# Optimization experiments

Hardware: AMD Instinct MI355X
Metric: run time of the kernel (lower is better)

The kernel has to match this reference:

```python
import jax, jax.numpy as jnp
import numpy as np

N_NODES = 50000
N_EDGES = 800000
IN_CH = 128
OUT_CH = 128
TIME_DIM = 64


def setup_inputs() -> dict:
    key = jax.random.key(0)
    ks = jax.random.split(key, 7)
    x = jax.random.normal(ks[0], (N_NODES, IN_CH), dtype=jnp.float32)
    edge_index = jax.random.randint(ks[1], (2, N_EDGES), 0, N_NODES, dtype=jnp.int64)
    edge_t = jax.random.uniform(ks[2], (N_EDGES,), dtype=jnp.float32)
    # parameters
    freqs = jax.random.normal(ks[3], (TIME_DIM // 2,), dtype=jnp.float32)
    fan = IN_CH + TIME_DIM
    lim = float(np.sqrt(1.0 / fan))
    lin_w = jax.random.uniform(ks[4], (OUT_CH, fan), minval=-lim, maxval=lim, dtype=jnp.float32)
    lin_b = jax.random.uniform(ks[5], (OUT_CH,), minval=-lim, maxval=lim, dtype=jnp.float32)
    glim = float(np.sqrt(6.0 / (1 + OUT_CH)))
    attn = jax.random.uniform(ks[6], (1, OUT_CH), minval=-glim, maxval=glim, dtype=jnp.float32)
    return {"x": x, "edge_index": edge_index, "edge_t": edge_t,
            "freqs": freqs, "lin_w": lin_w, "lin_b": lin_b, "attn": attn}


def reference(x, edge_index, edge_t, freqs, lin_w, lin_b, attn):
    src, dst = edge_index[0], edge_index[1]
    n_nodes = x.shape[0]
    # time encoding: [E, time_dim]
    ang = edge_t[:, None] * freqs * (2.0 * jnp.pi)
    edge_attr = jnp.concatenate([jnp.sin(ang), jnp.cos(ang)], axis=-1)
    # gather source features and project: h = tanh(Linear(cat(x_j, te)))
    msg = jnp.concatenate([x[src], edge_attr], axis=-1)        # [E, in+time]
    h = jnp.tanh(msg @ lin_w.T + lin_b)                        # [E, out]
    # segment softmax over destination nodes
    alpha = (h * attn).sum(axis=-1)                            # [E]
    seg_max = jax.ops.segment_max(alpha, dst, num_segments=n_nodes)
    ex = jnp.exp(alpha - seg_max[dst])
    denom = jax.ops.segment_sum(ex, dst, num_segments=n_nodes)
    w = ex / (denom[dst] + 1e-16)
    # scatter-add aggregation
    out = jax.ops.segment_sum(h * w[:, None], dst, num_segments=n_nodes)
    return out
```

## Files before the change

kernel.cpp:

```cpp
#include <hip/hip_runtime.h>
#include <hip/hip_bf16.h>
#include <math.h>

#define IN_CHN 128
#define OUT_CHN 128
#define KD 192
#define TM 64
#define HXP 136

typedef __bf16 bf16x8 __attribute__((ext_vector_type(8)));
typedef float f32x4 __attribute__((ext_vector_type(4)));

static __device__ __forceinline__ unsigned short f2b(float f) {
    return __builtin_bit_cast(unsigned short, (__bf16)f);
}
static __device__ __forceinline__ float b2f(unsigned short b) {
    return __uint_as_float(((unsigned int)b) << 16);
}
static __device__ __forceinline__ float fast_tanh(float x) {
    float e = __expf(2.0f * x);
    return 1.0f - 2.0f * __builtin_amdgcn_rcpf(e + 1.0f);
}

#define GLL16(gsrc, ldst) \
    __builtin_amdgcn_global_load_lds( \
        (const __attribute__((address_space(1))) unsigned int*)(gsrc), \
        (__attribute__((address_space(3))) unsigned int*)(ldst), 16, 0, 0)

#define LDS_BARRIER() do { \
    asm volatile("s_waitcnt lgkmcnt(0)" ::: "memory"); \
    __builtin_amdgcn_s_barrier(); \
    __builtin_amdgcn_sched_barrier(0); \
} while (0)


__global__ __launch_bounds__(256) void cvt_init(const float* __restrict__ x,
    unsigned short* __restrict__ xb, int* __restrict__ deg,
    int* __restrict__ side_node, long long n8, int Nn, int nb)
{
    long long i = (long long)blockIdx.x * 256 + threadIdx.x;
    if (i < n8) {
        const float4* src = (const float4*)(x + i * 8);
        float4 v0 = src[0], v1 = src[1];
        ushort4 p0 = { f2b(v0.x), f2b(v0.y), f2b(v0.z), f2b(v0.w) };
        ushort4 p1 = { f2b(v1.x), f2b(v1.y), f2b(v1.z), f2b(v1.w) };
        *(ushort4*)(xb + i * 8)     = p0;
        *(ushort4*)(xb + i * 8 + 4) = p1;
    }
    int t = (int)i;
    if (t < Nn) deg[t] = 0;
    if (t < nb) side_node[t] = -1;
}


__global__ __launch_bounds__(256) void count_deg(const int* __restrict__ ei,
                                                 int* __restrict__ deg, int E) {
    int e = blockIdx.x * 256 + threadIdx.x;
    if (e < E) atomicAdd(&deg[ei[E + e]], 1);
}

static __device__ __forceinline__ int wave_incl_scan(int v, int lane) {
    #pragma unroll
    for (int off = 1; off < 64; off <<= 1) {
        int t = __shfl_up(v, off);
        if (lane >= off) v += t;
    }
    return v;
}

__global__ __launch_bounds__(256) void scan_local(const int* __restrict__ deg,
    int* __restrict__ offs, int* __restrict__ partial, int Nn)
{
    __shared__ int wsum[4];
    int tid = threadIdx.x, lane = tid & 63, wid = tid >> 6;
    int i = blockIdx.x * 256 + tid;
    int v = (i < Nn) ? deg[i] : 0;
    int incl = wave_incl_scan(v, lane);
    if (lane == 63) wsum[wid] = incl;
    __syncthreads();
    int wpre = 0;
    for (int w = 0; w < wid; ++w) wpre += wsum[w];
    if (i < Nn) offs[i] = wpre + incl - v;
    if (tid == 255) partial[blockIdx.x] = wpre + incl;
}

__global__ __launch_bounds__(256) void finalize2(int* __restrict__ offs,
    const int* __restrict__ partial, int* __restrict__ cursor,
    int Nn, int E, int nblk)
{
    __shared__ int wsum[4];
    int b = blockIdx.x, tid = threadIdx.x, lane = tid & 63, wid = tid >> 6;
    int v = (tid < b && tid < nblk) ? partial[tid] : 0;
    #pragma unroll
    for (int off = 32; off > 0; off >>= 1) v += __shfl_xor(v, off);
    if (lane == 0) wsum[wid] = v;
    __syncthreads();
    int bp = wsum[0] + wsum[1] + wsum[2] + wsum[3];
    int i = b * 256 + tid;
    if (i < Nn) {
        int o = offs[i] + bp;
        offs[i] = o; cursor[i] = o;
        if (i == Nn - 1) offs[Nn] = E;
    }
}

__global__ __launch_bounds__(256) void fill_perm(const int* __restrict__ ei,
    const float* __restrict__ et, int* __restrict__ cursor,
    uint2* __restrict__ mt, int E)
{
    int e = blockIdx.x * 256 + threadIdx.x;
    if (e < E) {
        int d = ei[E + e];
        int pos = atomicAdd(&cursor[d], 1);
        mt[pos] = make_uint2((unsigned)ei[e], __float_as_uint(et[e]));
    }
}


__device__ __forceinline__ void load_meta(const uint2* __restrict__ mt,
    int tile, int E, int rbase, int g, int trow, int sv[2], float& tsv)
{
    int e0 = tile * TM;
    #pragma unroll
    for (int i = 0; i < 2; ++i) {
        int e = e0 + rbase + i * 4 + g;
        sv[i] = (int)mt[e < E ? e : E - 1].x;
    }
    int el = e0 + trow;
    tsv = __uint_as_float(mt[el < E ? el : E - 1].y);
}

__global__ __launch_bounds__(512) void gemm_fused(
    const unsigned short* __restrict__ xb, const uint2* __restrict__ mt,
    const int* __restrict__ offs,
    const float* __restrict__ freqs, const float* __restrict__ lw,
    const float* __restrict__ lb, const float* __restrict__ attn,
    float* __restrict__ out, float* __restrict__ den_g,
    int* __restrict__ side_node, float* __restrict__ side_den,
    float* __restrict__ side_val,
    int E, int Nn, int n_tiles, int kq, int kr)
{
    __shared__ unsigned short xs[2][TM][128];
    __shared__ __align__(16) unsigned short uni[TM * HXP + 128];
    unsigned short* te = uni;
    unsigned short* hx = uni;
    float* exs = (float*)(uni + TM * HXP);

    const int b    = blockIdx.x;
    const int t0   = b * kq + min(b, kr);
    const int cnt  = kq + (b < kr ? 1 : 0);
    if (cnt <= 0 || t0 >= n_tiles) return;
    const int tend = min(t0 + cnt, n_tiles);
    const int be0  = t0 * TM;
    const int bend = min(tend * TM, E);

    const int tid  = threadIdx.x;
    const int lane = tid & 63;
    const int wv   = tid >> 6;
    const int c16  = lane & 15;
    const int g    = lane >> 4;
    const int wbase = wv * 16;
    const int rbase = wv * 8;
    const int trow  = tid >> 3;
    const int tpart = tid & 7;
    const int sub  = lane >> 4;
    const int chl  = lane & 15;

    bf16x8 Wf[6];
    #pragma unroll
    for (int kk = 0; kk < 6; ++kk) {
        const float* wp = lw + (size_t)(wbase + c16) * KD + kk * 32 + g * 8;
        float4 v0 = *(const float4*)wp;
        float4 v1 = *(const float4*)(wp + 4);
        bf16x8 bb;
        bb[0] = (__bf16)v0.x; bb[1] = (__bf16)v0.y; bb[2] = (__bf16)v0.z; bb[3] = (__bf16)v0.w;
        bb[4] = (__bf16)v1.x; bb[5] = (__bf16)v1.y; bb[6] = (__bf16)v1.z; bb[7] = (__bf16)v1.w;
        Wf[kk] = bb;
    }
    const f32x4 bias_v = *(const f32x4*)(lb   + wbase + g * 4);
    const f32x4 attn_v = *(const f32x4*)(attn + wbase + g * 4);

    const float coff = (tpart >= 4) ? 1.5707963267948966f : 0.0f;
    float frv[8];
    #pragma unroll
    for (int j = 0; j < 8; ++j) frv[j] = freqs[(tpart & 3) * 8 + j] * 6.283185307179586f;

    int n0;
    {
        int lo = 0, hi = Nn;
        while (lo + 1 < hi) {
            int mid = (lo + hi) >> 1;
            if (offs[mid] <= be0) lo = mid; else hi = mid;
        }
        n0 = lo;
    }
    int cur_node = n0 + ((wv - (n0 & 7)) & 7);
    float a[8];
    #pragma unroll
    for (int q = 0; q < 8; ++q) a[q] = 0.0f;
    float den = 0.0f;

    float ts_cur, ts_nxt;
    int sv_nxt[2];
    {
        int sv0[2];
        load_meta(mt, t0, E, rbase, g, trow, sv0, ts_cur);
        #pragma unroll
        for (int i = 0; i < 2; ++i) {
            const int rlo = (rbase + i * 4 + g) & 15;
            const unsigned short* gsrc = xb + (size_t)sv0[i] * IN_CHN + ((c16 ^ rlo) * 8);
            GLL16(gsrc, &xs[0][rbase + i * 4][0]);
        }
        int t1 = t0 + 1;
        load_meta(mt, t1 < tend ? t1 : tend - 1, E, rbase, g, trow, sv_nxt, ts_nxt);
    }

    int cur = 0;
    for (int tile = t0; tile < tend; ++tile) {
        const int e0 = tile * TM;
        const int e1 = e0 + TM;

        ushort4 tp[2];
        {
            float v[8];
            #pragma unroll
            for (int j = 0; j < 8; ++j)
                v[j] = __sinf(ts_cur * frv[j] + coff);
            tp[0] = (ushort4){ f2b(v[0]), f2b(v[1]), f2b(v[2]), f2b(v[3]) };
            tp[1] = (ushort4){ f2b(v[4]), f2b(v[5]), f2b(v[6]), f2b(v[7]) };
        }
        int sv2[2]; float ts2;
        {
            int t2 = tile + 2;
            load_meta(mt, t2 < tend ? t2 : tend - 1, E, rbase, g, trow, sv2, ts2);
        }

        __syncthreads();

        if (tile + 1 < tend) {
            #pragma unroll
            for (int i = 0; i < 2; ++i) {
                const int rlo = (rbase + i * 4 + g) & 15;
                const unsigned short* gsrc = xb + (size_t)sv_nxt[i] * IN_CHN + ((c16 ^ rlo) * 8);
                GLL16(gsrc, &xs[cur ^ 1][rbase + i * 4][0]);
            }
        }
        {
            unsigned short* tr = &te[trow * 64];
            int slot = (tpart ^ (trow & 7)) * 8;
            *(ushort4*)(tr + slot)     = tp[0];
            *(ushort4*)(tr + slot + 4) = tp[1];
            if (tid < TM) exs[tid] = 0.0f;
        }

        LDS_BARRIER();

        f32x4 acc[4];
        #pragma unroll
        for (int mi = 0; mi < 4; ++mi) acc[mi] = (f32x4){0.f, 0.f, 0.f, 0.f};

        __builtin_amdgcn_s_setprio(1);
        const unsigned short* xsc = &xs[cur][0][0];
        #pragma unroll
        for (int mi = 0; mi < 4; ++mi) {
            const int r = mi * 16 + c16;
            const unsigned short* xrow = xsc + r * 128;
            #pragma unroll
            for (int kk = 0; kk < 4; ++kk) {
                const int slot = ((kk << 2) + g) ^ c16;
                bf16x8 av = __builtin_bit_cast(bf16x8, *(const uint4*)(xrow + slot * 8));
                acc[mi] = __builtin_amdgcn_mfma_f32_16x16x32_bf16(Wf[kk], av, acc[mi], 0, 0, 0);
            }
            const unsigned short* trw = &te[r * 64];
            bf16x8 s8 = __builtin_bit_cast(bf16x8, *(const uint4*)(trw + ((g ^ (r & 7)) * 8)));
            bf16x8 c8 = __builtin_bit_cast(bf16x8, *(const uint4*)(trw + (((g + 4) ^ (r & 7)) * 8)));
            acc[mi] = __builtin_amdgcn_mfma_f32_16x16x32_bf16(Wf[4], s8, acc[mi], 0, 0, 0);
            acc[mi] = __builtin_amdgcn_mfma_f32_16x16x32_bf16(Wf[5], c8, acc[mi], 0, 0, 0);
        }
        __builtin_amdgcn_s_setprio(0);

        LDS_BARRIER();

        #pragma unroll
        for (int mi = 0; mi < 4; ++mi) {
            const int r = mi * 16 + c16;
            f32x4 z = acc[mi];
            float p = 0.0f;
            #pragma unroll
            for (int q = 0; q < 4; ++q) {
                float h = fast_tanh(z[q] + bias_v[q]);
                z[q] = h;
                p = fmaf(h, attn_v[q], p);
            }
            ushort4 pv = (ushort4){ f2b(z[0]), f2b(z[1]), f2b(z[2]), f2b(z[3]) };
            *(ushort4*)&hx[r * HXP + wbase + g * 4] = pv;
            p += __shfl_xor(p, 16);
            p += __shfl_xor(p, 32);
            if (g == 0) atomicAdd(&exs[r], p);
        }

        LDS_BARRIER();

        while (cur_node < Nn) {
            int s  = offs[cur_node];
            if (s >= e1) break;
            int en = offs[cur_node + 1];
            int lo = s > e0 ? s : e0;
            int hi = en < e1 ? en : e1;
            for (int i = lo + sub; i < hi; i += 4) {
                int li = i - e0;
                float ex = __expf(exs[li]);
                uint4 hv = *(const uint4*)&hx[li * HXP + chl * 8];
                den += ex;
                unsigned int hw[4] = { hv.x, hv.y, hv.z, hv.w };
                #pragma unroll
                for (int q = 0; q < 4; ++q) {
                    a[2*q]   = fmaf(ex, b2f((unsigned short)(hw[q] & 0xFFFFu)), a[2*q]);
                    a[2*q+1] = fmaf(ex, b2f((unsigned short)(hw[q] >> 16)),     a[2*q+1]);
                }
            }
            if (en <= e1) {
                #pragma unroll
                for (int q = 0; q < 8; ++q) {
                    a[q] += __shfl_xor(a[q], 16);
                    a[q] += __shfl_xor(a[q], 32);
                }
                float ds = den + __shfl_xor(den, 16);
                ds += __shfl_xor(ds, 32);
                if (sub == 0) {
                    float* op = out + (size_t)cur_node * OUT_CHN + chl * 8;
                    *(float4*)op       = (float4){a[0], a[1], a[2], a[3]};
                    *(float4*)(op + 4) = (float4){a[4], a[5], a[6], a[7]};
                    if (chl == 0) den_g[cur_node] = ds;
                }
                #pragma unroll
                for (int q = 0; q < 8; ++q) a[q] = 0.0f;
                den = 0.0f;
                cur_node += 8;
            } else break;
        }

        ts_cur = ts_nxt; ts_nxt = ts2;
        sv_nxt[0] = sv2[0]; sv_nxt[1] = sv2[1];
        cur ^= 1;
    }

    if (cur_node < Nn) {
        int s = offs[cur_node];
        if (s < bend && offs[cur_node + 1] > bend) {
            #pragma unroll
            for (int q = 0; q < 8; ++q) {
                a[q] += __shfl_xor(a[q], 16);
                a[q] += __shfl_xor(a[q], 32);
            }
            float ds = den + __shfl_xor(den, 16);
            ds += __shfl_xor(ds, 32);
            if (sub == 0) {
                float* sv = side_val + (size_t)b * OUT_CHN + chl * 8;
                *(float4*)sv       = (float4){a[0], a[1], a[2], a[3]};
                *(float4*)(sv + 4) = (float4){a[4], a[5], a[6], a[7]};
                if (chl == 0) {
                    side_den[b] = ds;
                    side_node[b] = cur_node;
                }
            }
        }
    }
}


__global__ __launch_bounds__(256) void fixup(const int* __restrict__ side_node,
    const float* __restrict__ side_den, const float* __restrict__ side_val,
    float* __restrict__ out, float* __restrict__ den_g, int nb)
{
    int w = (blockIdx.x * 256 + threadIdx.x) >> 6;
    int lane = threadIdx.x & 63;
    if (w >= nb) return;
    int node = side_node[w];
    if (node < 0) return;
    const float* sv = side_val + (size_t)w * OUT_CHN;
    float* op = out + (size_t)node * OUT_CHN;
    atomicAdd(op + lane * 2,     sv[lane * 2]);
    atomicAdd(op + lane * 2 + 1, sv[lane * 2 + 1]);
    if (lane == 0) atomicAdd(&den_g[node], side_den[w]);
}


__global__ __launch_bounds__(256) void normalize(float* __restrict__ out,
    const float* __restrict__ den_g, const int* __restrict__ offs, int Nn)
{
    int gid = blockIdx.x * 256 + threadIdx.x;
    int n = gid >> 5;
    if (n >= Nn) return;
    int c = (gid & 31) * 4;
    float4* p = (float4*)(out + (size_t)n * OUT_CHN + c);
    if (offs[n + 1] == offs[n]) { *p = (float4){0, 0, 0, 0}; return; }
    float rs = __builtin_amdgcn_rcpf(den_g[n] + 1e-16f);
    float4 v = *p;
    v.x *= rs; v.y *= rs; v.z *= rs; v.w *= rs;
    *p = v;
}


extern "C" void kernel_launch(void* const* d_in, const int* in_sizes, int n_in,
                              void* d_out, int out_size, void* d_ws, size_t ws_size,
                              hipStream_t stream) {
    const float* x     = (const float*)d_in[0];
    const int*   ei    = (const int*)d_in[1];
    const float* et    = (const float*)d_in[2];
    const float* freqs = (const float*)d_in[3];
    const float* lw    = (const float*)d_in[4];
    const float* lb    = (const float*)d_in[5];
    const float* attn  = (const float*)d_in[6];
    float* out = (float*)d_out;

    const int E  = in_sizes[2];
    const int Nn = in_sizes[0] / IN_CHN;
    const int NB = 768;

    char* ws = (char*)d_ws;
    uint2* mt      = (uint2*)ws;         size_t off = (size_t)E * sizeof(uint2);
    unsigned short* xb = (unsigned short*)(ws + off); off += (size_t)Nn * IN_CHN * sizeof(unsigned short);
    float* den_g   = (float*)(ws + off); off += (size_t)Nn * sizeof(float);
    int*   deg     = (int*)(ws + off);   off += (size_t)Nn * sizeof(int);
    int*   offs    = (int*)(ws + off);   off += (size_t)(Nn + 1) * sizeof(int);
    int*   cursor  = (int*)(ws + off);   off += (size_t)Nn * sizeof(int);
    int*   partial = (int*)(ws + off);   off += 1024 * sizeof(int);
    int*   side_node = (int*)(ws + off); off += (size_t)NB * sizeof(int);
    float* side_den  = (float*)(ws + off); off += (size_t)NB * sizeof(float);
    float* side_val  = (float*)(ws + off);

    const int nblk = (Nn + 255) / 256;
    const int eblk = (E + 255) / 256;

    long long n8 = (long long)Nn * IN_CHN / 8;
    cvt_init<<<(unsigned)((n8 + 255) / 256), 256, 0, stream>>>(x, xb, deg, side_node, n8, Nn, NB);

    count_deg<<<eblk, 256, 0, stream>>>(ei, deg, E);
    scan_local<<<nblk, 256, 0, stream>>>(deg, offs, partial, Nn);
    finalize2<<<nblk, 256, 0, stream>>>(offs, partial, cursor, Nn, E, nblk);
    fill_perm<<<eblk, 256, 0, stream>>>(ei, et, cursor, mt, E);

    const int n_tiles = (E + TM - 1) / TM;
    const int kq = n_tiles / NB, kr = n_tiles % NB;
    gemm_fused<<<NB, 512, 0, stream>>>(xb, mt, offs, freqs, lw, lb, attn,
                                       out, den_g, side_node, side_den, side_val,
                                       E, Nn, n_tiles, kq, kr);

    fixup<<<(NB * 64 + 255) / 256, 256, 0, stream>>>(side_node, side_den, side_val,
                                                     out, den_g, NB);

    normalize<<<(Nn * 32 + 255) / 256, 256, 0, stream>>>(out, den_g, offs, Nn);
}
```

Measured before the change: 250.4 us.

## Double-buffer time-encoding and score LDS to drop two barriers per tile

The time-encoding tile and the per-edge score buffer are now double-buffered and no longer share memory with the bf16 h tile. The next tile's sin/cos encoding is computed and written one iteration ahead. This removes the barrier before the MFMA loop and the one between the MFMA loop and the tanh/hx write, so each tile needs fewer block-wide syncs. LDS use per block rises to about 66KB, and the grid is cut from 768 to 512 blocks to match the lower residency per CU.

```diff
diff --git a/kernel.cpp b/kernel.cpp
--- a/kernel.cpp
+++ b/kernel.cpp
@@ -141,10 +141,9 @@
     int E, int Nn, int n_tiles, int kq, int kr)
 {
     __shared__ unsigned short xs[2][TM][128];
-    __shared__ __align__(16) unsigned short uni[TM * HXP + 128];
-    unsigned short* te = uni;
-    unsigned short* hx = uni;
-    float* exs = (float*)(uni + TM * HXP);
+    __shared__ unsigned short te[2][TM * 64];
+    __shared__ unsigned short hx[TM * HXP];
+    __shared__ float exs[2][TM];
 
     const int b    = blockIdx.x;
     const int t0   = b * kq + min(b, kr);
@@ -200,17 +199,27 @@
     for (int q = 0; q < 8; ++q) a[q] = 0.0f;
     float den = 0.0f;
 
-    float ts_cur, ts_nxt;
+    float ts_nxt;
     int sv_nxt[2];
     {
-        int sv0[2];
-        load_meta(mt, t0, E, rbase, g, trow, sv0, ts_cur);
+        int sv0[2]; float ts0;
+        load_meta(mt, t0, E, rbase, g, trow, sv0, ts0);
         #pragma unroll
         for (int i = 0; i < 2; ++i) {
             const int rlo = (rbase + i * 4 + g) & 15;
             const unsigned short* gsrc = xb + (size_t)sv0[i] * IN_CHN + ((c16 ^ rlo) * 8);
             GLL16(gsrc, &xs[0][rbase + i * 4][0]);
         }
+        float v[8];
+        #pragma unroll
+        for (int j = 0; j < 8; ++j)
+            v[j] = __sinf(ts0 * frv[j] + coff);
+        unsigned short* tr = &te[0][trow * 64];
+        int slot = (tpart ^ (trow & 7)) * 8;
+        *(ushort4*)(tr + slot)     = (ushort4){ f2b(v[0]), f2b(v[1]), f2b(v[2]), f2b(v[3]) };
+        *(ushort4*)(tr + slot + 4) = (ushort4){ f2b(v[4]), f2b(v[5]), f2b(v[6]), f2b(v[7]) };
+        if (tid < TM) exs[0][tid] = 0.0f;
+
         int t1 = t0 + 1;
         load_meta(mt, t1 < tend ? t1 : tend - 1, E, rbase, g, trow, sv_nxt, ts_nxt);
     }
@@ -220,14 +229,15 @@
         const int e0 = tile * TM;
         const int e1 = e0 + TM;
 
-        ushort4 tp[2];
         {
             float v[8];
             #pragma unroll
             for (int j = 0; j < 8; ++j)
-                v[j] = __sinf(ts_cur * frv[j] + coff);
-            tp[0] = (ushort4){ f2b(v[0]), f2b(v[1]), f2b(v[2]), f2b(v[3]) };
-            tp[1] = (ushort4){ f2b(v[4]), f2b(v[5]), f2b(v[6]), f2b(v[7]) };
+                v[j] = __sinf(ts_nxt * frv[j] + coff);
+            unsigned short* tr = &te[cur ^ 1][trow * 64];
+            int slot = (tpart ^ (trow & 7)) * 8;
+            *(ushort4*)(tr + slot)     = (ushort4){ f2b(v[0]), f2b(v[1]), f2b(v[2]), f2b(v[3]) };
+            *(ushort4*)(tr + slot + 4) = (ushort4){ f2b(v[4]), f2b(v[5]), f2b(v[6]), f2b(v[7]) };
         }
         int sv2[2]; float ts2;
         {
@@ -245,15 +255,7 @@
                 GLL16(gsrc, &xs[cur ^ 1][rbase + i * 4][0]);
             }
         }
-        {
-            unsigned short* tr = &te[trow * 64];
-            int slot = (tpart ^ (trow & 7)) * 8;
-            *(ushort4*)(tr + slot)     = tp[0];
-            *(ushort4*)(tr + slot + 4) = tp[1];
-            if (tid < TM) exs[tid] = 0.0f;
-        }
-
-        LDS_BARRIER();
+        if (tid < TM) exs[cur ^ 1][tid] = 0.0f;
 
         f32x4 acc[4];
         #pragma unroll
@@ -261,6 +263,7 @@
 
         __builtin_amdgcn_s_setprio(1);
         const unsigned short* xsc = &xs[cur][0][0];
+        const unsigned short* tec = &te[cur][0];
         #pragma unroll
         for (int mi = 0; mi < 4; ++mi) {
             const int r = mi * 16 + c16;
@@ -271,15 +274,13 @@
                 bf16x8 av = __builtin_bit_cast(bf16x8, *(const uint4*)(xrow + slot * 8));
                 acc[mi] = __builtin_amdgcn_mfma_f32_16x16x32_bf16(Wf[kk], av, acc[mi], 0, 0, 0);
             }
-            const unsigned short* trw = &te[r * 64];
+            const unsigned short* trw = tec + r * 64;
             bf16x8 s8 = __builtin_bit_cast(bf16x8, *(const uint4*)(trw + ((g ^ (r & 7)) * 8)));
             bf16x8 c8 = __builtin_bit_cast(bf16x8, *(const uint4*)(trw + (((g + 4) ^ (r & 7)) * 8)));
             acc[mi] = __builtin_amdgcn_mfma_f32_16x16x32_bf16(Wf[4], s8, acc[mi], 0, 0, 0);
             acc[mi] = __builtin_amdgcn_mfma_f32_16x16x32_bf16(Wf[5], c8, acc[mi], 0, 0, 0);
         }
         __builtin_amdgcn_s_setprio(0);
-
-        LDS_BARRIER();
 
         #pragma unroll
         for (int mi = 0; mi < 4; ++mi) {
@@ -296,7 +297,7 @@
             *(ushort4*)&hx[r * HXP + wbase + g * 4] = pv;
             p += __shfl_xor(p, 16);
             p += __shfl_xor(p, 32);
-            if (g == 0) atomicAdd(&exs[r], p);
+            if (g == 0) atomicAdd(&exs[cur][r], p);
         }
 
         LDS_BARRIER();
@@ -309,7 +310,7 @@
             int hi = en < e1 ? en : e1;
             for (int i = lo + sub; i < hi; i += 4) {
                 int li = i - e0;
-                float ex = __expf(exs[li]);
+                float ex = __expf(exs[cur][li]);
                 uint4 hv = *(const uint4*)&hx[li * HXP + chl * 8];
                 den += ex;
                 unsigned int hw[4] = { hv.x, hv.y, hv.z, hv.w };
@@ -340,7 +341,7 @@
             } else break;
         }
 
-        ts_cur = ts_nxt; ts_nxt = ts2;
+        ts_nxt = ts2;
         sv_nxt[0] = sv2[0]; sv_nxt[1] = sv2[1];
         cur ^= 1;
     }
@@ -416,7 +417,7 @@
 
     const int E  = in_sizes[2];
     const int Nn = in_sizes[0] / IN_CHN;
-    const int NB = 768;
+    const int NB = 512;
 
     char* ws = (char*)d_ws;
     uint2* mt      = (uint2*)ws;         size_t off = (size_t)E * sizeof(uint2);
```

Measured after the change: 234.7 us. 1.07x faster.
